# Kernel optimization log

Measured on AMD Instinct MI355X. Metric: run time of the kernel, lower is better.

The kernel has to match this reference:

```python
import jax, jax.numpy as jnp
import numpy as np

N_QUBITS = 10
DEPTH = 2
CNOT_PATTERN = [(i, i + 1) for i in range(N_QUBITS - 1)] + [(N_QUBITS - 1, 0)]

def _signs(n):
    # Pauli-Z eigenvalue (+1/-1) of each basis state for each wire; wire 0 = MSB
    idx = np.arange(2 ** n)
    bits = (idx[:, None] >> np.arange(n - 1, -1, -1)[None, :]) & 1
    return jnp.asarray(1.0 - 2.0 * bits, jnp.float32)  # [2^n, n]

SIGNS = _signs(N_QUBITS)

def _apply_rx(s, theta, wire):
    # s: [B, 2,2,...,2] complex; RX(theta) = [[c, -i s],[-i s, c]], c=cos(theta/2)
    s0 = jnp.take(s, 0, axis=wire + 1)
    s1 = jnp.take(s, 1, axis=wire + 1)
    c = jnp.cos(theta * 0.5)
    sn = jnp.sin(theta * 0.5)
    if c.ndim:  # per-batch angle -> broadcast over remaining wire axes
        shp = (-1,) + (1,) * (s0.ndim - 1)
        c = c.reshape(shp)
        sn = sn.reshape(shp)
    return jnp.stack([c * s0 - 1j * sn * s1, -1j * sn * s0 + c * s1], axis=wire + 1)

def _apply_cnot(s, src, tgt):
    # flip target wire on the src=1 subspace (X gate == flip of the size-2 axis)
    s0 = jnp.take(s, 0, axis=src + 1)
    s1 = jnp.take(s, 1, axis=src + 1)
    t_ax = tgt + 1 - (1 if tgt > src else 0)  # target axis after removing src axis
    s1 = jnp.flip(s1, axis=t_ax)
    return jnp.stack([s0, s1], axis=src + 1)

def _qgate(x, rx_params):
    # x: [B, n_qubits] data angles -> PauliZ expectations [B, n_qubits]
    B = x.shape[0]
    n = N_QUBITS
    s = jnp.zeros((B, 2 ** n), jnp.complex64).at[:, 0].set(1.0)
    s = s.reshape((B,) + (2,) * n)
    for w in range(n):
        s = _apply_rx(s, x[:, w], w)
    for _ in range(DEPTH):
        for w in range(n):
            s = _apply_rx(s, rx_params[w], w)
        for src, tgt in CNOT_PATTERN:
            s = _apply_cnot(s, src, tgt)
    probs = jnp.abs(s.reshape(B, -1)) ** 2  # [B, 2^n]
    return probs @ SIGNS  # [B, n]


def setup_inputs():
    key = jax.random.key(0)
    ks = jax.random.split(key, 10)
    T, B, D, H = 256, 256, 128, N_QUBITS
    fan_in = D + H
    sc = 1.0 / np.sqrt(fan_in)
    def lin(k1, k2):
        W = jax.random.uniform(k1, (H, fan_in), jnp.float32, -sc, sc)
        b = jax.random.uniform(k2, (H,), jnp.float32, -sc, sc)
        return W, b
    inputs = jax.random.normal(ks[0], (T, B, D), jnp.float32)
    rx_params = jax.random.normal(ks[1], (H,), jnp.float32)
    Wf, bf = lin(ks[2], ks[3])
    Wi, bi = lin(ks[4], ks[5])
    Wg, bg = lin(ks[6], ks[7])
    Wo, bo = lin(ks[8], ks[9])
    return dict(inputs=inputs, rx_params=rx_params, Wf=Wf, bf=bf, Wi=Wi, bi=bi,
                Wg=Wg, bg=bg, Wo=Wo, bo=bo)


def reference(inputs, rx_params, Wf, bf, Wi, bi, Wg, bg, Wo, bo):
    T, B, _ = inputs.shape
    H = N_QUBITS
    def step(carry, x_t):
        hx, cx = carry
        comb = jnp.concatenate([x_t, hx], axis=1)  # [B, D+H]
        f = jax.nn.sigmoid(_qgate(comb @ Wf.T + bf, rx_params))
        i = jax.nn.sigmoid(_qgate(comb @ Wi.T + bi, rx_params))
        g = jnp.tanh(_qgate(comb @ Wg.T + bg, rx_params))
        o = jax.nn.sigmoid(_qgate(comb @ Wo.T + bo, rx_params))
        cx = f * cx + i * g
        hx = o * jnp.tanh(cx)
        return (hx, cx), hx
    h0 = jnp.zeros((B, H), inputs.dtype)
    c0 = jnp.zeros((B, H), inputs.dtype)
    (hT, cT), ys = jax.lax.scan(step, (h0, c0), inputs)
    return ys, hT, cT
```

## Files before the change

kernel.cpp:

```cpp
#include <hip/hip_runtime.h>
#include <math.h>

#define T_STEPS 256
#define BATCH   256
#define DDIM    128
#define NH      10

typedef float v2f __attribute__((ext_vector_type(2)));

__device__ __forceinline__ v2f sp(float x){ v2f r; r.x = x; r.y = x; return r; }
#define PKFMA(a,b,c) __builtin_elementwise_fma((a),(b),(c))

template<int CTRL, int RMASK, int BMASK>
__device__ __forceinline__ float dppz(float x){
  return __int_as_float(__builtin_amdgcn_update_dpp(
      0, __float_as_int(x), CTRL, RMASK, BMASK, true));
}
template<int CTRL>
__device__ __forceinline__ float qperm(float x){
  int xi = __float_as_int(x);
  return __int_as_float(__builtin_amdgcn_update_dpp(xi, xi, CTRL, 0xF, 0xF, false));
}
__device__ __forceinline__ float red63(float v){
  v += dppz<0x111, 0xF, 0xF>(v);
  v += dppz<0x112, 0xF, 0xF>(v);
  v += dppz<0x114, 0xF, 0xE>(v);
  v += dppz<0x118, 0xF, 0xC>(v);
  v += dppz<0x142, 0xA, 0xF>(v);
  v += dppz<0x143, 0xC, 0xF>(v);
  return v;
}
__device__ __forceinline__ float wave_sum_b(float v){
  return __int_as_float(__builtin_amdgcn_readlane(__float_as_int(red63(v)), 63));
}
__device__ __forceinline__ float qp2(float x){ return qperm<0x4E>(x); }
__device__ __forceinline__ float qp1(float x){ return qperm<0xB1>(x); }

template<int CTRL, int RMASK, int BMASK>
__device__ __forceinline__ float lad_add(float v){ return v + dppz<CTRL,RMASK,BMASK>(v); }
template<int CTRL, int RMASK, int BMASK>
__device__ __forceinline__ float lad_sub(float v){ return dppz<CTRL,RMASK,BMASK>(v) - v; }

#define LAD0_A(v) lad_add<0x111,0xF,0xF>(v)
#define LAD0_S(v) lad_sub<0x111,0xF,0xF>(v)
#define LAD1_A(v) lad_add<0x112,0xF,0xF>(v)
#define LAD1_S(v) lad_sub<0x112,0xF,0xF>(v)
#define LAD2_A(v) lad_add<0x114,0xF,0xE>(v)
#define LAD2_S(v) lad_sub<0x114,0xF,0xE>(v)
#define LAD3_A(v) lad_add<0x118,0xF,0xC>(v)
#define LAD3_S(v) lad_sub<0x118,0xF,0xC>(v)
#define LAD4_A(v) lad_add<0x142,0xA,0xF>(v)
#define LAD4_S(v) lad_sub<0x142,0xA,0xF>(v)
#define LAD5_A(v) lad_add<0x143,0xC,0xF>(v)
#define LAD5_S(v) lad_sub<0x143,0xC,0xF>(v)

__device__ __forceinline__ float dsx32(float x){ return __shfl_xor(x, 32, 64); }
__device__ __forceinline__ float dsx16(float x){
  return __int_as_float(__builtin_amdgcn_ds_swizzle(__float_as_int(x), 0x401F));
}
__device__ __forceinline__ float dsx8(float x){
  return __int_as_float(__builtin_amdgcn_ds_swizzle(__float_as_int(x), 0x201F));
}
__device__ __forceinline__ float dsx4(float x){
  return __int_as_float(__builtin_amdgcn_ds_swizzle(__float_as_int(x), 0x101F));
}

#define NK 4

#define RX_LANE_PK(FETCH, cv, sv)                                              \
  { const v2f cc_ = sp(cv), ss_ = sp(sv);                                      \
    _Pragma("unroll")                                                          \
    for (int k = 0; k < NK; ++k){                                              \
      v2f oa, ob;                                                              \
      oa.x = FETCH(RE[k].x); oa.y = FETCH(RE[k].y);                            \
      ob.x = FETCH(IM[k].x); ob.y = FETCH(IM[k].y);                            \
      RE[k] = PKFMA(cc_, RE[k], ss_ * ob);                                     \
      IM[k] = PKFMA(cc_, IM[k], -(ss_ * oa));                                  \
    } }

template<int XB>
__device__ __forceinline__ void rx_reg_pk(float c, float s, v2f* RE, v2f* IM){
  const v2f cc = sp(c), ss = sp(s);
  v2f oR[NK], oI[NK];
  #pragma unroll
  for (int k = 0; k < NK; ++k){ oR[k] = RE[k]; oI[k] = IM[k]; }
  #pragma unroll
  for (int k = 0; k < NK; ++k){
    RE[k] = PKFMA(cc, oR[k],  ss * oI[k ^ XB]);
    IM[k] = PKFMA(cc, oI[k], -(ss * oR[k ^ XB]));
  }
}
__device__ __forceinline__ void rx_reg9_pk(float c, float s, v2f* RE, v2f* IM){
  const v2f cc = sp(c), ss = sp(s);
  #pragma unroll
  for (int k = 0; k < NK; ++k){
    v2f oa = __builtin_shufflevector(RE[k], RE[k], 1, 0);
    v2f ob = __builtin_shufflevector(IM[k], IM[k], 1, 0);
    RE[k] = PKFMA(cc, RE[k],  ss * ob);
    IM[k] = PKFMA(cc, IM[k], -(ss * oa));
  }
}

__global__ void __launch_bounds__(512)
__attribute__((amdgpu_waves_per_eu(2)))
qlstm_kernel(const float* __restrict__ inp, const float* __restrict__ rxp,
             const float* __restrict__ Wf, const float* __restrict__ bf,
             const float* __restrict__ Wi, const float* __restrict__ bi,
             const float* __restrict__ Wg, const float* __restrict__ bg,
             const float* __restrict__ Wo, const float* __restrict__ bo,
             float* __restrict__ out)
{
  const int b    = blockIdx.x;
  const int tid  = threadIdx.x;
  const int wv   = tid >> 6;
  const int g    = wv >> 1;
  const int half = wv & 1;
  const int lane = tid & 63;

  __shared__ float4 Sx[4][2][4][64];
  __shared__ float4 partv[2][64];
  __shared__ float2 csn[4][2][5];
  ((float*)partv)[tid] = 0.f;

  const float* Wp = (g == 0) ? Wf : (g == 1) ? Wi : (g == 2) ? Wg : Wo;
  const float* bp = (g == 0) ? bf : (g == 1) ? bi : (g == 2) ? bg : bo;

  const float WSC = 0.07957747154594767f;
  v2f WA[5], WB[5], WC[5];
  float bT[NH];
  #pragma unroll
  for (int j = 0; j < 5; ++j){
    const int w0 = 2*j, w1 = 2*j + 1;
    WA[j].x = WSC * Wp[w0*138 + lane];        WA[j].y = WSC * Wp[w1*138 + lane];
    WB[j].x = WSC * Wp[w0*138 + 64 + lane];   WB[j].y = WSC * Wp[w1*138 + 64 + lane];
    WC[j].x = (lane < NH) ? WSC * Wp[w0*138 + 128 + lane] : 0.f;
    WC[j].y = (lane < NH) ? WSC * Wp[w1*138 + 128 + lane] : 0.f;
  }
  #pragma unroll
  for (int w = 0; w < NH; ++w) bT[w] = WSC * (bp[w] + rxp[w]);

  float pc[NH], ps[NH];
  #pragma unroll
  for (int w = 0; w < NH; ++w){
    float th = 0.5f * rxp[w];
    pc[w] = cosf(th);
    ps[w] = sinf(th);
  }

  const int l5 = (lane>>5)&1, l4 = (lane>>4)&1, l3 = (lane>>3)&1;
  const int l2 = (lane>>2)&1, l1 = (lane>>1)&1, l0 = lane&1;
  const int pb2 = l4^l3, pb3 = l3^l2, pb4 = l2^l1, pb5 = l1^l0;
  const int a0 = l5, a1 = l5^l4;
  const int a6w = l0 ^ half;
  const int n_base = pb2 + pb3 + pb4 + pb5 + a6w;

  v2f CRE[NK], CIM[NK];
  #pragma unroll
  for (int r = 0; r < 2*NK; ++r){
    const int R0 = r&1, R1 = (r>>1)&1, R2 = (r>>2)&1;
    int k = (n_base + (a0^R0) + (a1^R0) + (half^R2) + (R2^R1) + (R1^R0)) & 3;
    float cr = (k==0) ? 1.f : (k==2) ? -1.f : 0.f;
    float ci = (k==1) ? -1.f : (k==3) ? 1.f : 0.f;
    if (R0){ CRE[r>>1].y = cr; CIM[r>>1].y = ci; }
    else   { CRE[r>>1].x = cr; CIM[r>>1].x = ci; }
  }

  const float sig = (lane == 0 || lane >= 6) ? -1.f : 1.f;

  float h = 0.f, c = 0.f;

  const float* x0 = inp + (size_t)b * DDIM;
  float xa = x0[lane];
  float xb = x0[64 + lane];

  __syncthreads();

  #pragma unroll 1
  for (int t = 0; t < T_STEPS; ++t){
    float xaC = xa, xbC = xb;
    if (t + 1 < T_STEPS){
      const float* nx = inp + ((size_t)(t+1) * BATCH + b) * DDIM;
      xa = nx[lane];
      xb = nx[64 + lane];
    }

    float cs[NH], sn[NH];
    {
      const v2f xav = sp(xaC), xbv = sp(xbC), hv = sp(h);
      if (half == 0){
        v2f p0 = PKFMA(xav, WA[0], PKFMA(xbv, WB[0], hv * WC[0]));
        v2f p1 = PKFMA(xav, WA[1], PKFMA(xbv, WB[1], hv * WC[1]));
        v2f p2 = PKFMA(xav, WA[2], PKFMA(xbv, WB[2], hv * WC[2]));
        float t0 = bT[0] + wave_sum_b(p0.x);
        float t1 = bT[1] + wave_sum_b(p0.y);
        float t2 = bT[2] + wave_sum_b(p1.x);
        float t3 = bT[3] + wave_sum_b(p1.y);
        float t4 = bT[4] + wave_sum_b(p2.x);
        cs[0] = __builtin_amdgcn_cosf(t0); sn[0] = __builtin_amdgcn_sinf(t0);
        cs[1] = __builtin_amdgcn_cosf(t1); sn[1] = __builtin_amdgcn_sinf(t1);
        cs[2] = __builtin_amdgcn_cosf(t2); sn[2] = __builtin_amdgcn_sinf(t2);
        cs[3] = __builtin_amdgcn_cosf(t3); sn[3] = __builtin_amdgcn_sinf(t3);
        cs[4] = __builtin_amdgcn_cosf(t4); sn[4] = __builtin_amdgcn_sinf(t4);
        if (lane == 0){
          csn[g][0][0] = make_float2(cs[0], sn[0]);
          csn[g][0][1] = make_float2(cs[1], sn[1]);
          csn[g][0][2] = make_float2(cs[2], sn[2]);
          csn[g][0][3] = make_float2(cs[3], sn[3]);
          csn[g][0][4] = make_float2(cs[4], sn[4]);
        }
      } else {
        v2f p2 = PKFMA(xav, WA[2], PKFMA(xbv, WB[2], hv * WC[2]));
        v2f p3 = PKFMA(xav, WA[3], PKFMA(xbv, WB[3], hv * WC[3]));
        v2f p4 = PKFMA(xav, WA[4], PKFMA(xbv, WB[4], hv * WC[4]));
        float t5 = bT[5] + wave_sum_b(p2.y);
        float t6 = bT[6] + wave_sum_b(p3.x);
        float t7 = bT[7] + wave_sum_b(p3.y);
        float t8 = bT[8] + wave_sum_b(p4.x);
        float t9 = bT[9] + wave_sum_b(p4.y);
        cs[5] = __builtin_amdgcn_cosf(t5); sn[5] = __builtin_amdgcn_sinf(t5);
        cs[6] = __builtin_amdgcn_cosf(t6); sn[6] = __builtin_amdgcn_sinf(t6);
        cs[7] = __builtin_amdgcn_cosf(t7); sn[7] = __builtin_amdgcn_sinf(t7);
        cs[8] = __builtin_amdgcn_cosf(t8); sn[8] = __builtin_amdgcn_sinf(t8);
        cs[9] = __builtin_amdgcn_cosf(t9); sn[9] = __builtin_amdgcn_sinf(t9);
        if (lane == 0){
          csn[g][1][0] = make_float2(cs[5], sn[5]);
          csn[g][1][1] = make_float2(cs[6], sn[6]);
          csn[g][1][2] = make_float2(cs[7], sn[7]);
          csn[g][1][3] = make_float2(cs[8], sn[8]);
          csn[g][1][4] = make_float2(cs[9], sn[9]);
        }
      }
    }
    __syncthreads();
    if (half == 0){
      float2 o0 = csn[g][1][0]; cs[5] = o0.x; sn[5] = o0.y;
      float2 o1 = csn[g][1][1]; cs[6] = o1.x; sn[6] = o1.y;
      float2 o2 = csn[g][1][2]; cs[7] = o2.x; sn[7] = o2.y;
      float2 o3 = csn[g][1][3]; cs[8] = o3.x; sn[8] = o3.y;
      float2 o4 = csn[g][1][4]; cs[9] = o4.x; sn[9] = o4.y;
    } else {
      float2 o0 = csn[g][0][0]; cs[0] = o0.x; sn[0] = o0.y;
      float2 o1 = csn[g][0][1]; cs[1] = o1.x; sn[1] = o1.y;
      float2 o2 = csn[g][0][2]; cs[2] = o2.x; sn[2] = o2.y;
      float2 o3 = csn[g][0][3]; cs[3] = o3.x; sn[3] = o3.y;
      float2 o4 = csn[g][0][4]; cs[4] = o4.x; sn[4] = o4.y;
    }

    float f2 = pb2 ? sn[2] : cs[2];
    float f3 = pb3 ? sn[3] : cs[3];
    float f4 = pb4 ? sn[4] : cs[4];
    float f5 = pb5 ? sn[5] : cs[5];
    float m2345 = ((f2*f3)*(f4*f5)) * (a6w ? sn[6] : cs[6]);

    float q0 = (a0 ? sn[0] : cs[0]) * (a1 ? sn[1] : cs[1]);
    float q1 = (a0 ? cs[0] : sn[0]) * (a1 ? cs[1] : sn[1]);
    v2f ZZ; ZZ.x = m2345 * q0; ZZ.y = m2345 * q1;

    float u7  = half ? sn[7] : cs[7];
    float u7b = half ? cs[7] : sn[7];
    float t78[4];
    t78[0] = u7  * cs[8];
    t78[1] = u7  * sn[8];
    t78[2] = u7b * sn[8];
    t78[3] = u7b * cs[8];

    v2f s9a; s9a.x = cs[9]; s9a.y = sn[9];
    v2f s9b; s9b.x = sn[9]; s9b.y = cs[9];

    v2f RE[NK], IM[NK];
    #pragma unroll
    for (int k = 0; k < NK; ++k){
      v2f M = (sp(t78[k]) * ((k & 1) ? s9b : s9a)) * ZZ;
      RE[k] = M * CRE[k];
      IM[k] = M * CIM[k];
    }

    RX_LANE_PK(dsx32, pc[0], ps[0])
    RX_LANE_PK(dsx16, pc[1], ps[1])
    RX_LANE_PK(dsx8,  pc[2], ps[2])
    RX_LANE_PK(dsx4,  pc[3], ps[3])
    RX_LANE_PK(qp2,   pc[4], ps[4])
    RX_LANE_PK(qp1,   pc[5], ps[5])
    rx_reg_pk<2>(pc[7], ps[7], RE, IM);
    rx_reg_pk<1>(pc[8], ps[8], RE, IM);
    rx_reg9_pk  (pc[9], ps[9], RE, IM);

    Sx[g][half][0][lane] = make_float4(RE[0].x, RE[0].y, RE[1].x, RE[1].y);
    Sx[g][half][1][lane] = make_float4(RE[2].x, RE[2].y, RE[3].x, RE[3].y);
    Sx[g][half][2][lane] = make_float4(IM[0].x, IM[0].y, IM[1].x, IM[1].y);
    Sx[g][half][3][lane] = make_float4(IM[2].x, IM[2].y, IM[3].x, IM[3].y);
    __syncthreads();
    {
      float4 pr0 = Sx[g][half^1][0][lane];
      float4 pr1 = Sx[g][half^1][1][lane];
      float4 pi0 = Sx[g][half^1][2][lane];
      float4 pi1 = Sx[g][half^1][3][lane];
      v2f PR[NK], PI[NK];
      PR[0].x = pr0.x; PR[0].y = pr0.y; PR[1].x = pr0.z; PR[1].y = pr0.w;
      PR[2].x = pr1.x; PR[2].y = pr1.y; PR[3].x = pr1.z; PR[3].y = pr1.w;
      PI[0].x = pi0.x; PI[0].y = pi0.y; PI[1].x = pi0.z; PI[1].y = pi0.w;
      PI[2].x = pi1.x; PI[2].y = pi1.y; PI[3].x = pi1.z; PI[3].y = pi1.w;
      const v2f c6 = sp(pc[6]), s6 = sp(ps[6]);
      #pragma unroll
      for (int k = 0; k < NK; ++k){
        RE[k] = PKFMA(c6, RE[k],  s6 * PI[k]);
        IM[k] = PKFMA(c6, IM[k], -(s6 * PR[k]));
      }
    }

    v2f Pk[NK];
    #pragma unroll
    for (int k = 0; k < NK; ++k) Pk[k] = PKFMA(RE[k], RE[k], IM[k] * IM[k]);
    float A0 = Pk[0].x + Pk[0].y, A1 = Pk[1].x + Pk[1].y;
    float A2 = Pk[2].x + Pk[2].y, A3 = Pk[3].x + Pk[3].y;
    float B0 = Pk[0].x - Pk[0].y, B1 = Pk[1].x - Pk[1].y;
    float B2 = Pk[2].x - Pk[2].y, B3 = Pk[3].x - Pk[3].y;
    float su = A0 + A1, sv = A2 + A3;
    float tot = su + sv;
    float q4  = su - sv;
    float q6  = (A0 - A1) - (A2 - A3);
    float q7  = (B0 - B1) - (B2 - B3);

    float a0p = LAD0_A(tot);
    float a0m = LAD0_S(tot);
    float b1pp = LAD1_A(a0p);
    float b1pm = LAD1_S(a0p);
    float b1mm = LAD1_S(a0m);
    float c2ppp = LAD2_A(b1pp);
    float c2ppm = LAD2_S(b1pp);
    float c2pmm = LAD2_S(b1pm);
    float c2mmm = LAD2_S(b1mm);
    float d1 = LAD3_A(c2ppp);
    float d2 = LAD3_S(c2ppp);
    float d3 = LAD3_S(c2ppm);
    float d4 = LAD3_S(c2pmm);
    float d5 = LAD3_S(c2mmm);
    float P1 = LAD5_S(LAD4_S(d1));
    float P2 = LAD5_S(LAD4_S(d2));
    float P3 = LAD5_S(LAD4_S(d3));
    float P4 = LAD5_S(LAD4_S(d4));
    float P5 = LAD5_S(LAD4_S(d5));
    float e = LAD0_S(q7);
    e = LAD1_S(e); e = LAD2_S(e); e = LAD3_S(e); e = LAD4_S(e);
    float P9 = LAD5_S(e);
    float P0 = LAD5_A(e);
    float f_ = LAD0_S(q4);
    f_ = LAD1_S(f_); f_ = LAD2_S(f_); f_ = LAD3_S(f_); f_ = LAD4_S(f_);
    float P7 = LAD5_S(f_);
    float g_ = LAD0_S(q6);
    g_ = LAD1_S(g_); g_ = LAD2_S(g_); g_ = LAD3_S(g_); g_ = LAD4_S(g_);
    float P8 = LAD5_S(g_);

    if (lane == 63){
      float vals[10] = {P0,P1,P2,P3,P4,P5,P5,P7,P8,P9};
      #pragma unroll
      for (int j = 0; j < 10; ++j)
        ((float*)&partv[half][j])[g] = vals[j];
    }
    __syncthreads();

    float4 eL = partv[0][lane];
    float4 eH = partv[1][lane];
    float E0 = fmaf(sig, eH.x, eL.x);
    float E1 = fmaf(sig, eH.y, eL.y);
    float E2 = fmaf(sig, eH.z, eL.z);
    float E3 = fmaf(sig, eH.w, eL.w);
    float fv = 1.f / (1.f + __expf(-E0));
    float iv = 1.f / (1.f + __expf(-E1));
    float e2g = __expf(2.f * E2);
    float gv = (e2g - 1.f) / (e2g + 1.f);
    float ov = 1.f / (1.f + __expf(-E3));
    c = fmaf(fv, c, iv * gv);
    float e2c = __expf(2.f * c);
    h = ov * ((e2c - 1.f) / (e2c + 1.f));

    if (wv == 0 && lane < NH)
      out[((size_t)t * BATCH + b) * NH + lane] = h;
  }

  if (wv == 0 && lane < NH){
    const size_t ysN = (size_t)T_STEPS * BATCH * NH;
    out[ysN + (size_t)b * NH + lane]                      = h;
    out[ysN + (size_t)BATCH * NH + (size_t)b * NH + lane] = c;
  }
}

extern "C" void kernel_launch(void* const* d_in, const int* in_sizes, int n_in,
                              void* d_out, int out_size, void* d_ws, size_t ws_size,
                              hipStream_t stream)
{
  qlstm_kernel<<<BATCH, 512, 0, stream>>>(
      (const float*)d_in[0], (const float*)d_in[1],
      (const float*)d_in[2], (const float*)d_in[3],
      (const float*)d_in[4], (const float*)d_in[5],
      (const float*)d_in[6], (const float*)d_in[7],
      (const float*)d_in[8], (const float*)d_in[9],
      (float*)d_out);
}
```

Baseline: 916.8 us.

## Split each gate's statevector across four waves with 1024-thread blocks

Each gate's 1024-amplitude state is now spread over four waves instead of two, so each lane keeps 8 amplitudes instead of 16. Qubits 6 and 7 become cross-wave and are applied together through one LDS exchange with the three partner waves. The per-wave angle projections use a shared shuffle-and-select reduction tree over 2–3 outputs instead of separate full wave sums. This halves per-wave register and ALU work and adds parallelism, at the cost of more LDS traffic and more threads per block in a serial recurrence.

```diff
diff --git a/kernel.cpp b/kernel.cpp
--- a/kernel.cpp
+++ b/kernel.cpp
@@ -7,7 +7,6 @@
 #define NH      10
 
 typedef float v2f __attribute__((ext_vector_type(2)));
-
 __device__ __forceinline__ v2f sp(float x){ v2f r; r.x = x; r.y = x; return r; }
 #define PKFMA(a,b,c) __builtin_elementwise_fma((a),(b),(c))
 
@@ -21,26 +20,17 @@
   int xi = __float_as_int(x);
   return __int_as_float(__builtin_amdgcn_update_dpp(xi, xi, CTRL, 0xF, 0xF, false));
 }
-__device__ __forceinline__ float red63(float v){
-  v += dppz<0x111, 0xF, 0xF>(v);
-  v += dppz<0x112, 0xF, 0xF>(v);
-  v += dppz<0x114, 0xF, 0xE>(v);
-  v += dppz<0x118, 0xF, 0xC>(v);
-  v += dppz<0x142, 0xA, 0xF>(v);
-  v += dppz<0x143, 0xC, 0xF>(v);
-  return v;
-}
-__device__ __forceinline__ float wave_sum_b(float v){
-  return __int_as_float(__builtin_amdgcn_readlane(__float_as_int(red63(v)), 63));
-}
 __device__ __forceinline__ float qp2(float x){ return qperm<0x4E>(x); }
 __device__ __forceinline__ float qp1(float x){ return qperm<0xB1>(x); }
 
-template<int CTRL, int RMASK, int BMASK>
+__device__ __forceinline__ float rdlane(float v, int l){
+  return __int_as_float(__builtin_amdgcn_readlane(__float_as_int(v), l));
+}
+
+template<int CTRL,int RMASK,int BMASK>
 __device__ __forceinline__ float lad_add(float v){ return v + dppz<CTRL,RMASK,BMASK>(v); }
-template<int CTRL, int RMASK, int BMASK>
+template<int CTRL,int RMASK,int BMASK>
 __device__ __forceinline__ float lad_sub(float v){ return dppz<CTRL,RMASK,BMASK>(v) - v; }
-
 #define LAD0_A(v) lad_add<0x111,0xF,0xF>(v)
 #define LAD0_S(v) lad_sub<0x111,0xF,0xF>(v)
 #define LAD1_A(v) lad_add<0x112,0xF,0xF>(v)
@@ -65,7 +55,39 @@
   return __int_as_float(__builtin_amdgcn_ds_swizzle(__float_as_int(x), 0x101F));
 }
 
-#define NK 4
+__device__ __forceinline__ void tree3(float v0, float v1, float v2,
+                                      int l5, int l4,
+                                      float& t0, float& t1, float& t2){
+  float a = v0 + dsx32(v0);
+  float b = v1 + dsx32(v1);
+  float c = v2 + dsx32(v2);
+  float m = l5 ? b : a;
+  m += dsx16(m);
+  c += dsx16(c);
+  float m2 = l4 ? c : m;
+  m2 += dsx8(m2);
+  m2 += dsx4(m2);
+  m2 += qp2(m2);
+  m2 += qp1(m2);
+  t0 = rdlane(m2, 0);
+  t1 = rdlane(m2, 32);
+  t2 = rdlane(m2, 16);
+}
+__device__ __forceinline__ void tree2(float v0, float v1, int l5,
+                                      float& t0, float& t1){
+  float a = v0 + dsx32(v0);
+  float b = v1 + dsx32(v1);
+  float m = l5 ? b : a;
+  m += dsx16(m);
+  m += dsx8(m);
+  m += dsx4(m);
+  m += qp2(m);
+  m += qp1(m);
+  t0 = rdlane(m, 0);
+  t1 = rdlane(m, 32);
+}
+
+#define NK 2
 
 #define RX_LANE_PK(FETCH, cv, sv)                                              \
   { const v2f cc_ = sp(cv), ss_ = sp(sv);                                      \
@@ -78,17 +100,13 @@
       IM[k] = PKFMA(cc_, IM[k], -(ss_ * oa));                                  \
     } }
 
-template<int XB>
-__device__ __forceinline__ void rx_reg_pk(float c, float s, v2f* RE, v2f* IM){
+__device__ __forceinline__ void rx_reg8_pk(float c, float s, v2f* RE, v2f* IM){
   const v2f cc = sp(c), ss = sp(s);
-  v2f oR[NK], oI[NK];
-  #pragma unroll
-  for (int k = 0; k < NK; ++k){ oR[k] = RE[k]; oI[k] = IM[k]; }
-  #pragma unroll
-  for (int k = 0; k < NK; ++k){
-    RE[k] = PKFMA(cc, oR[k],  ss * oI[k ^ XB]);
-    IM[k] = PKFMA(cc, oI[k], -(ss * oR[k ^ XB]));
-  }
+  v2f oR0 = RE[0], oI0 = IM[0], oR1 = RE[1], oI1 = IM[1];
+  RE[0] = PKFMA(cc, oR0,  ss * oI1);
+  IM[0] = PKFMA(cc, oI0, -(ss * oR1));
+  RE[1] = PKFMA(cc, oR1,  ss * oI0);
+  IM[1] = PKFMA(cc, oI1, -(ss * oR0));
 }
 __device__ __forceinline__ void rx_reg9_pk(float c, float s, v2f* RE, v2f* IM){
   const v2f cc = sp(c), ss = sp(s);
@@ -101,8 +119,8 @@
   }
 }
 
-__global__ void __launch_bounds__(512)
-__attribute__((amdgpu_waves_per_eu(2)))
+__global__ void __launch_bounds__(1024)
+__attribute__((amdgpu_waves_per_eu(4)))
 qlstm_kernel(const float* __restrict__ inp, const float* __restrict__ rxp,
              const float* __restrict__ Wf, const float* __restrict__ bf,
              const float* __restrict__ Wi, const float* __restrict__ bi,
@@ -113,31 +131,35 @@
   const int b    = blockIdx.x;
   const int tid  = threadIdx.x;
   const int wv   = tid >> 6;
-  const int g    = wv >> 1;
-  const int half = wv & 1;
+  const int g    = wv >> 2;
+  const int q    = wv & 3;
+  const int W1   = (q >> 1) & 1;
+  const int W0   = q & 1;
   const int lane = tid & 63;
 
-  __shared__ float4 Sx[4][2][4][64];
-  __shared__ float4 partv[2][64];
-  __shared__ float2 csn[4][2][5];
+  __shared__ float4 Sx[4][4][2][64];
+  __shared__ float4 partv[4][64];
+  __shared__ float4 csn4[4][5];
   ((float*)partv)[tid] = 0.f;
 
   const float* Wp = (g == 0) ? Wf : (g == 1) ? Wi : (g == 2) ? Wg : Wo;
   const float* bp = (g == 0) ? bf : (g == 1) ? bi : (g == 2) ? bg : bo;
 
+  const int cnt   = (q < 2) ? 3 : 2;
+  const int wbase = (q < 2) ? 3*q : 6 + 2*(q - 2);
+
   const float WSC = 0.07957747154594767f;
-  v2f WA[5], WB[5], WC[5];
-  float bT[NH];
+  float wa[3], wb[3], wc[3], bq[3];
   #pragma unroll
-  for (int j = 0; j < 5; ++j){
-    const int w0 = 2*j, w1 = 2*j + 1;
-    WA[j].x = WSC * Wp[w0*138 + lane];        WA[j].y = WSC * Wp[w1*138 + lane];
-    WB[j].x = WSC * Wp[w0*138 + 64 + lane];   WB[j].y = WSC * Wp[w1*138 + 64 + lane];
-    WC[j].x = (lane < NH) ? WSC * Wp[w0*138 + 128 + lane] : 0.f;
-    WC[j].y = (lane < NH) ? WSC * Wp[w1*138 + 128 + lane] : 0.f;
-  }
-  #pragma unroll
-  for (int w = 0; w < NH; ++w) bT[w] = WSC * (bp[w] + rxp[w]);
+  for (int j = 0; j < 3; ++j){
+    if (j < cnt){
+      const int w = wbase + j;
+      wa[j] = WSC * Wp[w*138 + lane];
+      wb[j] = WSC * Wp[w*138 + 64 + lane];
+      wc[j] = (lane < NH) ? WSC * Wp[w*138 + 128 + lane] : 0.f;
+      bq[j] = WSC * (bp[w] + rxp[w]);
+    } else { wa[j] = wb[j] = wc[j] = bq[j] = 0.f; }
+  }
 
   float pc[NH], ps[NH];
   #pragma unroll
@@ -146,26 +168,31 @@
     pc[w] = cosf(th);
     ps[w] = sinf(th);
   }
+  const float cc67 = pc[6]*pc[7], cs67 = pc[6]*ps[7];
+  const float sc67 = ps[6]*pc[7], ss67 = ps[6]*ps[7];
 
   const int l5 = (lane>>5)&1, l4 = (lane>>4)&1, l3 = (lane>>3)&1;
   const int l2 = (lane>>2)&1, l1 = (lane>>1)&1, l0 = lane&1;
   const int pb2 = l4^l3, pb3 = l3^l2, pb4 = l2^l1, pb5 = l1^l0;
   const int a0 = l5, a1 = l5^l4;
-  const int a6w = l0 ^ half;
+  const int a6w = l0 ^ W1;
+  const int w17 = W1 ^ W0;
   const int n_base = pb2 + pb3 + pb4 + pb5 + a6w;
 
   v2f CRE[NK], CIM[NK];
   #pragma unroll
   for (int r = 0; r < 2*NK; ++r){
-    const int R0 = r&1, R1 = (r>>1)&1, R2 = (r>>2)&1;
-    int k = (n_base + (a0^R0) + (a1^R0) + (half^R2) + (R2^R1) + (R1^R0)) & 3;
+    const int R0 = r&1, R1 = (r>>1)&1;
+    int k = (n_base + (a0^R0) + (a1^R0) + w17 + (W0^R1) + (R1^R0)) & 3;
     float cr = (k==0) ? 1.f : (k==2) ? -1.f : 0.f;
     float ci = (k==1) ? -1.f : (k==3) ? 1.f : 0.f;
     if (R0){ CRE[r>>1].y = cr; CIM[r>>1].y = ci; }
     else   { CRE[r>>1].x = cr; CIM[r>>1].x = ci; }
   }
 
-  const float sig = (lane == 0 || lane >= 6) ? -1.f : 1.f;
+  const float sg1 = (lane == 0 || lane >= 7) ? -1.f : 1.f;
+  const float sg2 = (lane == 0 || lane >= 6) ? -1.f : 1.f;
+  const float sg3 = (lane == 6) ? -1.f : 1.f;
 
   float h = 0.f, c = 0.f;
 
@@ -184,66 +211,34 @@
       xb = nx[64 + lane];
     }
 
+    {
+      float v0 = fmaf(xaC, wa[0], fmaf(xbC, wb[0], h * wc[0]));
+      float v1 = fmaf(xaC, wa[1], fmaf(xbC, wb[1], h * wc[1]));
+      float t0, t1, t2 = 0.f;
+      if (cnt == 3){
+        float v2 = fmaf(xaC, wa[2], fmaf(xbC, wb[2], h * wc[2]));
+        tree3(v0, v1, v2, l5, l4, t0, t1, t2);
+      } else {
+        tree2(v0, v1, l5, t0, t1);
+      }
+      t0 += bq[0]; t1 += bq[1]; t2 += bq[2];
+      float c0 = __builtin_amdgcn_cosf(t0), s0 = __builtin_amdgcn_sinf(t0);
+      float c1 = __builtin_amdgcn_cosf(t1), s1 = __builtin_amdgcn_sinf(t1);
+      float c2 = __builtin_amdgcn_cosf(t2), s2 = __builtin_amdgcn_sinf(t2);
+      if (lane == 0){
+        float2* c2p = (float2*)&csn4[g][0];
+        c2p[wbase]     = make_float2(c0, s0);
+        c2p[wbase + 1] = make_float2(c1, s1);
+        if (cnt == 3) c2p[wbase + 2] = make_float2(c2, s2);
+      }
+    }
+    __syncthreads();
     float cs[NH], sn[NH];
-    {
-      const v2f xav = sp(xaC), xbv = sp(xbC), hv = sp(h);
-      if (half == 0){
-        v2f p0 = PKFMA(xav, WA[0], PKFMA(xbv, WB[0], hv * WC[0]));
-        v2f p1 = PKFMA(xav, WA[1], PKFMA(xbv, WB[1], hv * WC[1]));
-        v2f p2 = PKFMA(xav, WA[2], PKFMA(xbv, WB[2], hv * WC[2]));
-        float t0 = bT[0] + wave_sum_b(p0.x);
-        float t1 = bT[1] + wave_sum_b(p0.y);
-        float t2 = bT[2] + wave_sum_b(p1.x);
-        float t3 = bT[3] + wave_sum_b(p1.y);
-        float t4 = bT[4] + wave_sum_b(p2.x);
-        cs[0] = __builtin_amdgcn_cosf(t0); sn[0] = __builtin_amdgcn_sinf(t0);
-        cs[1] = __builtin_amdgcn_cosf(t1); sn[1] = __builtin_amdgcn_sinf(t1);
-        cs[2] = __builtin_amdgcn_cosf(t2); sn[2] = __builtin_amdgcn_sinf(t2);
-        cs[3] = __builtin_amdgcn_cosf(t3); sn[3] = __builtin_amdgcn_sinf(t3);
-        cs[4] = __builtin_amdgcn_cosf(t4); sn[4] = __builtin_amdgcn_sinf(t4);
-        if (lane == 0){
-          csn[g][0][0] = make_float2(cs[0], sn[0]);
-          csn[g][0][1] = make_float2(cs[1], sn[1]);
-          csn[g][0][2] = make_float2(cs[2], sn[2]);
-          csn[g][0][3] = make_float2(cs[3], sn[3]);
-          csn[g][0][4] = make_float2(cs[4], sn[4]);
-        }
-      } else {
-        v2f p2 = PKFMA(xav, WA[2], PKFMA(xbv, WB[2], hv * WC[2]));
-        v2f p3 = PKFMA(xav, WA[3], PKFMA(xbv, WB[3], hv * WC[3]));
-        v2f p4 = PKFMA(xav, WA[4], PKFMA(xbv, WB[4], hv * WC[4]));
-        float t5 = bT[5] + wave_sum_b(p2.y);
-        float t6 = bT[6] + wave_sum_b(p3.x);
-        float t7 = bT[7] + wave_sum_b(p3.y);
-        float t8 = bT[8] + wave_sum_b(p4.x);
-        float t9 = bT[9] + wave_sum_b(p4.y);
-        cs[5] = __builtin_amdgcn_cosf(t5); sn[5] = __builtin_amdgcn_sinf(t5);
-        cs[6] = __builtin_amdgcn_cosf(t6); sn[6] = __builtin_amdgcn_sinf(t6);
-        cs[7] = __builtin_amdgcn_cosf(t7); sn[7] = __builtin_amdgcn_sinf(t7);
-        cs[8] = __builtin_amdgcn_cosf(t8); sn[8] = __builtin_amdgcn_sinf(t8);
-        cs[9] = __builtin_amdgcn_cosf(t9); sn[9] = __builtin_amdgcn_sinf(t9);
-        if (lane == 0){
-          csn[g][1][0] = make_float2(cs[5], sn[5]);
-          csn[g][1][1] = make_float2(cs[6], sn[6]);
-          csn[g][1][2] = make_float2(cs[7], sn[7]);
-          csn[g][1][3] = make_float2(cs[8], sn[8]);
-          csn[g][1][4] = make_float2(cs[9], sn[9]);
-        }
-      }
-    }
-    __syncthreads();
-    if (half == 0){
-      float2 o0 = csn[g][1][0]; cs[5] = o0.x; sn[5] = o0.y;
-      float2 o1 = csn[g][1][1]; cs[6] = o1.x; sn[6] = o1.y;
-      float2 o2 = csn[g][1][2]; cs[7] = o2.x; sn[7] = o2.y;
-      float2 o3 = csn[g][1][3]; cs[8] = o3.x; sn[8] = o3.y;
-      float2 o4 = csn[g][1][4]; cs[9] = o4.x; sn[9] = o4.y;
-    } else {
-      float2 o0 = csn[g][0][0]; cs[0] = o0.x; sn[0] = o0.y;
-      float2 o1 = csn[g][0][1]; cs[1] = o1.x; sn[1] = o1.y;
-      float2 o2 = csn[g][0][2]; cs[2] = o2.x; sn[2] = o2.y;
-      float2 o3 = csn[g][0][3]; cs[3] = o3.x; sn[3] = o3.y;
-      float2 o4 = csn[g][0][4]; cs[4] = o4.x; sn[4] = o4.y;
+    #pragma unroll
+    for (int j = 0; j < 5; ++j){
+      float4 cw = csn4[g][j];
+      cs[2*j]   = cw.x; sn[2*j]   = cw.y;
+      cs[2*j+1] = cw.z; sn[2*j+1] = cw.w;
     }
 
     float f2 = pb2 ? sn[2] : cs[2];
@@ -256,23 +251,18 @@
     float q1 = (a0 ? cs[0] : sn[0]) * (a1 ? cs[1] : sn[1]);
     v2f ZZ; ZZ.x = m2345 * q0; ZZ.y = m2345 * q1;
 
-    float u7  = half ? sn[7] : cs[7];
-    float u7b = half ? cs[7] : sn[7];
-    float t78[4];
-    t78[0] = u7  * cs[8];
-    t78[1] = u7  * sn[8];
-    t78[2] = u7b * sn[8];
-    t78[3] = u7b * cs[8];
-
+    float f7  = w17 ? sn[7] : cs[7];
+    float t8a = f7 * (W0 ? sn[8] : cs[8]);
+    float t8b = f7 * (W0 ? cs[8] : sn[8]);
     v2f s9a; s9a.x = cs[9]; s9a.y = sn[9];
     v2f s9b; s9b.x = sn[9]; s9b.y = cs[9];
 
     v2f RE[NK], IM[NK];
-    #pragma unroll
-    for (int k = 0; k < NK; ++k){
-      v2f M = (sp(t78[k]) * ((k & 1) ? s9b : s9a)) * ZZ;
-      RE[k] = M * CRE[k];
-      IM[k] = M * CIM[k];
+    {
+      v2f M0 = (sp(t8a) * s9a) * ZZ;
+      v2f M1 = (sp(t8b) * s9b) * ZZ;
+      RE[0] = M0 * CRE[0]; IM[0] = M0 * CIM[0];
+      RE[1] = M1 * CRE[1]; IM[1] = M1 * CIM[1];
     }
 
     RX_LANE_PK(dsx32, pc[0], ps[0])
@@ -281,45 +271,43 @@
     RX_LANE_PK(dsx4,  pc[3], ps[3])
     RX_LANE_PK(qp2,   pc[4], ps[4])
     RX_LANE_PK(qp1,   pc[5], ps[5])
-    rx_reg_pk<2>(pc[7], ps[7], RE, IM);
-    rx_reg_pk<1>(pc[8], ps[8], RE, IM);
-    rx_reg9_pk  (pc[9], ps[9], RE, IM);
-
-    Sx[g][half][0][lane] = make_float4(RE[0].x, RE[0].y, RE[1].x, RE[1].y);
-    Sx[g][half][1][lane] = make_float4(RE[2].x, RE[2].y, RE[3].x, RE[3].y);
-    Sx[g][half][2][lane] = make_float4(IM[0].x, IM[0].y, IM[1].x, IM[1].y);
-    Sx[g][half][3][lane] = make_float4(IM[2].x, IM[2].y, IM[3].x, IM[3].y);
+    rx_reg8_pk(pc[8], ps[8], RE, IM);
+    rx_reg9_pk(pc[9], ps[9], RE, IM);
+
+    Sx[g][q][0][lane] = make_float4(RE[0].x, RE[0].y, RE[1].x, RE[1].y);
+    Sx[g][q][1][lane] = make_float4(IM[0].x, IM[0].y, IM[1].x, IM[1].y);
     __syncthreads();
     {
-      float4 pr0 = Sx[g][half^1][0][lane];
-      float4 pr1 = Sx[g][half^1][1][lane];
-      float4 pi0 = Sx[g][half^1][2][lane];
-      float4 pi1 = Sx[g][half^1][3][lane];
-      v2f PR[NK], PI[NK];
-      PR[0].x = pr0.x; PR[0].y = pr0.y; PR[1].x = pr0.z; PR[1].y = pr0.w;
-      PR[2].x = pr1.x; PR[2].y = pr1.y; PR[3].x = pr1.z; PR[3].y = pr1.w;
-      PI[0].x = pi0.x; PI[0].y = pi0.y; PI[1].x = pi0.z; PI[1].y = pi0.w;
-      PI[2].x = pi1.x; PI[2].y = pi1.y; PI[3].x = pi1.z; PI[3].y = pi1.w;
-      const v2f c6 = sp(pc[6]), s6 = sp(ps[6]);
+      float4 r1 = Sx[g][q^1][0][lane], i1 = Sx[g][q^1][1][lane];
+      float4 r2 = Sx[g][q^2][0][lane], i2 = Sx[g][q^2][1][lane];
+      float4 r3 = Sx[g][q^3][0][lane], i3 = Sx[g][q^3][1][lane];
+      v2f R1v[2], I1v[2], R2v[2], I2v[2], R3v[2], I3v[2];
+      R1v[0].x = r1.x; R1v[0].y = r1.y; R1v[1].x = r1.z; R1v[1].y = r1.w;
+      I1v[0].x = i1.x; I1v[0].y = i1.y; I1v[1].x = i1.z; I1v[1].y = i1.w;
+      R2v[0].x = r2.x; R2v[0].y = r2.y; R2v[1].x = r2.z; R2v[1].y = r2.w;
+      I2v[0].x = i2.x; I2v[0].y = i2.y; I2v[1].x = i2.z; I2v[1].y = i2.w;
+      R3v[0].x = r3.x; R3v[0].y = r3.y; R3v[1].x = r3.z; R3v[1].y = r3.w;
+      I3v[0].x = i3.x; I3v[0].y = i3.y; I3v[1].x = i3.z; I3v[1].y = i3.w;
+      const v2f vcc = sp(cc67), vcs = sp(cs67), vsc = sp(sc67), vss = sp(ss67);
       #pragma unroll
       for (int k = 0; k < NK; ++k){
-        RE[k] = PKFMA(c6, RE[k],  s6 * PI[k]);
-        IM[k] = PKFMA(c6, IM[k], -(s6 * PR[k]));
+        v2f nre = PKFMA(vcc, RE[k],
+                  PKFMA(vcs, I1v[k],
+                  PKFMA(vsc, I2v[k], -(vss * R3v[k]))));
+        v2f nim = PKFMA(vcc, IM[k],
+                  -(PKFMA(vcs, R1v[k],
+                    PKFMA(vsc, R2v[k], vss * I3v[k]))));
+        RE[k] = nre; IM[k] = nim;
       }
     }
 
-    v2f Pk[NK];
-    #pragma unroll
-    for (int k = 0; k < NK; ++k) Pk[k] = PKFMA(RE[k], RE[k], IM[k] * IM[k]);
-    float A0 = Pk[0].x + Pk[0].y, A1 = Pk[1].x + Pk[1].y;
-    float A2 = Pk[2].x + Pk[2].y, A3 = Pk[3].x + Pk[3].y;
-    float B0 = Pk[0].x - Pk[0].y, B1 = Pk[1].x - Pk[1].y;
-    float B2 = Pk[2].x - Pk[2].y, B3 = Pk[3].x - Pk[3].y;
-    float su = A0 + A1, sv = A2 + A3;
-    float tot = su + sv;
-    float q4  = su - sv;
-    float q6  = (A0 - A1) - (A2 - A3);
-    float q7  = (B0 - B1) - (B2 - B3);
+    v2f Pk0 = PKFMA(RE[0], RE[0], IM[0]*IM[0]);
+    v2f Pk1 = PKFMA(RE[1], RE[1], IM[1]*IM[1]);
+    float A0 = Pk0.x + Pk0.y, A1 = Pk1.x + Pk1.y;
+    float B0 = Pk0.x - Pk0.y, B1 = Pk1.x - Pk1.y;
+    float tot = A0 + A1;
+    float qA  = A0 - A1;
+    float qB  = B0 - B1;
 
     float a0p = LAD0_A(tot);
     float a0m = LAD0_S(tot);
@@ -340,31 +328,30 @@
     float P3 = LAD5_S(LAD4_S(d3));
     float P4 = LAD5_S(LAD4_S(d4));
     float P5 = LAD5_S(LAD4_S(d5));
-    float e = LAD0_S(q7);
+    float e = LAD0_S(qB);
     e = LAD1_S(e); e = LAD2_S(e); e = LAD3_S(e); e = LAD4_S(e);
     float P9 = LAD5_S(e);
     float P0 = LAD5_A(e);
-    float f_ = LAD0_S(q4);
+    float f_ = LAD0_S(qA);
     f_ = LAD1_S(f_); f_ = LAD2_S(f_); f_ = LAD3_S(f_); f_ = LAD4_S(f_);
-    float P7 = LAD5_S(f_);
-    float g_ = LAD0_S(q6);
-    g_ = LAD1_S(g_); g_ = LAD2_S(g_); g_ = LAD3_S(g_); g_ = LAD4_S(g_);
-    float P8 = LAD5_S(g_);
+    float P8 = LAD5_S(f_);
 
     if (lane == 63){
-      float vals[10] = {P0,P1,P2,P3,P4,P5,P5,P7,P8,P9};
+      float vals[10] = {P0, P1, P2, P3, P4, P5, P5, P5, P8, P9};
       #pragma unroll
       for (int j = 0; j < 10; ++j)
-        ((float*)&partv[half][j])[g] = vals[j];
+        ((float*)&partv[q][j])[g] = vals[j];
     }
     __syncthreads();
 
-    float4 eL = partv[0][lane];
-    float4 eH = partv[1][lane];
-    float E0 = fmaf(sig, eH.x, eL.x);
-    float E1 = fmaf(sig, eH.y, eL.y);
-    float E2 = fmaf(sig, eH.z, eL.z);
-    float E3 = fmaf(sig, eH.w, eL.w);
+    float4 e0 = partv[0][lane];
+    float4 e1 = partv[1][lane];
+    float4 e2 = partv[2][lane];
+    float4 e3 = partv[3][lane];
+    float E0 = fmaf(sg3, e3.x, fmaf(sg2, e2.x, fmaf(sg1, e1.x, e0.x)));
+    float E1 = fmaf(sg3, e3.y, fmaf(sg2, e2.y, fmaf(sg1, e1.y, e0.y)));
+    float E2 = fmaf(sg3, e3.z, fmaf(sg2, e2.z, fmaf(sg1, e1.z, e0.z)));
+    float E3 = fmaf(sg3, e3.w, fmaf(sg2, e2.w, fmaf(sg1, e1.w, e0.w)));
     float fv = 1.f / (1.f + __expf(-E0));
     float iv = 1.f / (1.f + __expf(-E1));
     float e2g = __expf(2.f * E2);
@@ -389,7 +376,7 @@
                               void* d_out, int out_size, void* d_ws, size_t ws_size,
                               hipStream_t stream)
 {
-  qlstm_kernel<<<BATCH, 512, 0, stream>>>(
+  qlstm_kernel<<<BATCH, 1024, 0, stream>>>(
       (const float*)d_in[0], (const float*)d_in[1],
       (const float*)d_in[2], (const float*)d_in[3],
       (const float*)d_in[4], (const float*)d_in[5],
```

New measurement: 1.050 ms. +14.5%, slower.

## Precompute next-step input projections early and drop one barrier per step

Applied to the files above, without the earlier changes.

The input-dependent part of the gate pre-activations for step t+1 is now computed during step t, while the state vector is being exchanged. Each half-wave computes and publishes its 5 input dot products through shared memory at the existing barrier. The small h-dependent part (10 terms) is computed per lane with readlane broadcasts, and cos/sin are evaluated once per lane and then broadcast, which removes the csn shared exchange and one __syncthreads per step. The cost is extra readlanes per step and a reordering of the recurrence that shortens the serial critical path.

```diff
diff --git a/kernel.cpp b/kernel.cpp
--- a/kernel.cpp
+++ b/kernel.cpp
@@ -7,7 +7,6 @@
 #define NH      10
 
 typedef float v2f __attribute__((ext_vector_type(2)));
-
 __device__ __forceinline__ v2f sp(float x){ v2f r; r.x = x; r.y = x; return r; }
 #define PKFMA(a,b,c) __builtin_elementwise_fma((a),(b),(c))
 
@@ -30,17 +29,16 @@
   v += dppz<0x143, 0xC, 0xF>(v);
   return v;
 }
-__device__ __forceinline__ float wave_sum_b(float v){
-  return __int_as_float(__builtin_amdgcn_readlane(__float_as_int(red63(v)), 63));
+__device__ __forceinline__ float rdlane(float v, int l){
+  return __int_as_float(__builtin_amdgcn_readlane(__float_as_int(v), l));
 }
 __device__ __forceinline__ float qp2(float x){ return qperm<0x4E>(x); }
 __device__ __forceinline__ float qp1(float x){ return qperm<0xB1>(x); }
 
-template<int CTRL, int RMASK, int BMASK>
+template<int CTRL,int RMASK,int BMASK>
 __device__ __forceinline__ float lad_add(float v){ return v + dppz<CTRL,RMASK,BMASK>(v); }
-template<int CTRL, int RMASK, int BMASK>
+template<int CTRL,int RMASK,int BMASK>
 __device__ __forceinline__ float lad_sub(float v){ return dppz<CTRL,RMASK,BMASK>(v) - v; }
-
 #define LAD0_A(v) lad_add<0x111,0xF,0xF>(v)
 #define LAD0_S(v) lad_sub<0x111,0xF,0xF>(v)
 #define LAD1_A(v) lad_add<0x112,0xF,0xF>(v)
@@ -99,6 +97,17 @@
     RE[k] = PKFMA(cc, RE[k],  ss * ob);
     IM[k] = PKFMA(cc, IM[k], -(ss * oa));
   }
+}
+
+__device__ __forceinline__ void xdots(float xa, float xb,
+                                      const v2f* WA, const v2f* WB, float* s){
+  v2f xav = sp(xa), xbv = sp(xb);
+  v2f p0 = PKFMA(xav, WA[0], xbv * WB[0]);
+  v2f p1 = PKFMA(xav, WA[1], xbv * WB[1]);
+  v2f p2 = PKFMA(xav, WA[2], xbv * WB[2]);
+  s[0] = red63(p0.x); s[1] = red63(p0.y);
+  s[2] = red63(p1.x); s[3] = red63(p1.y);
+  s[4] = red63(p2.x);
 }
 
 __global__ void __launch_bounds__(512)
@@ -119,25 +128,38 @@
 
   __shared__ float4 Sx[4][2][4][64];
   __shared__ float4 partv[2][64];
-  __shared__ float2 csn[4][2][5];
+  __shared__ float xpub_s[4][16];
   ((float*)partv)[tid] = 0.f;
 
   const float* Wp = (g == 0) ? Wf : (g == 1) ? Wi : (g == 2) ? Wg : Wo;
   const float* bp = (g == 0) ? bf : (g == 1) ? bi : (g == 2) ? bg : bo;
 
   const float WSC = 0.07957747154594767f;
-  v2f WA[5], WB[5], WC[5];
-  float bT[NH];
-  #pragma unroll
-  for (int j = 0; j < 5; ++j){
-    const int w0 = 2*j, w1 = 2*j + 1;
-    WA[j].x = WSC * Wp[w0*138 + lane];        WA[j].y = WSC * Wp[w1*138 + lane];
-    WB[j].x = WSC * Wp[w0*138 + 64 + lane];   WB[j].y = WSC * Wp[w1*138 + 64 + lane];
-    WC[j].x = (lane < NH) ? WSC * Wp[w0*138 + 128 + lane] : 0.f;
-    WC[j].y = (lane < NH) ? WSC * Wp[w1*138 + 128 + lane] : 0.f;
-  }
-  #pragma unroll
-  for (int w = 0; w < NH; ++w) bT[w] = WSC * (bp[w] + rxp[w]);
+
+  const int wbase = half * 5;
+  v2f WA[3], WB[3];
+  float bq[5];
+  #pragma unroll
+  for (int k = 0; k < 5; ++k) bq[k] = WSC * (bp[wbase + k] + rxp[wbase + k]);
+  #pragma unroll
+  for (int j = 0; j < 3; ++j){
+    const int w0 = wbase + 2*j, w1 = wbase + 2*j + 1;
+    WA[j].x = WSC * Wp[w0*138 + lane];
+    WB[j].x = WSC * Wp[w0*138 + 64 + lane];
+    if (2*j + 1 < 5){
+      WA[j].y = WSC * Wp[w1*138 + lane];
+      WB[j].y = WSC * Wp[w1*138 + 64 + lane];
+    } else { WA[j].y = 0.f; WB[j].y = 0.f; }
+  }
+  float wCT[NH];
+  {
+    const int row = (lane < NH) ? lane : 0;
+    #pragma unroll
+    for (int j = 0; j < NH; ++j){
+      float v = WSC * Wp[row*138 + 128 + j];
+      wCT[j] = (lane < NH) ? v : 0.f;
+    }
+  }
 
   float pc[NH], ps[NH];
   #pragma unroll
@@ -173,11 +195,18 @@
   float xa = x0[lane];
   float xb = x0[64 + lane];
 
+  {
+    float sx[5];
+    xdots(xa, xb, WA, WB, sx);
+    if (lane == 63){
+      #pragma unroll
+      for (int k = 0; k < 5; ++k) xpub_s[g][wbase + k] = sx[k] + bq[k];
+    }
+  }
   __syncthreads();
 
   #pragma unroll 1
   for (int t = 0; t < T_STEPS; ++t){
-    float xaC = xa, xbC = xb;
     if (t + 1 < T_STEPS){
       const float* nx = inp + ((size_t)(t+1) * BATCH + b) * DDIM;
       xa = nx[lane];
@@ -186,64 +215,25 @@
 
     float cs[NH], sn[NH];
     {
-      const v2f xav = sp(xaC), xbv = sp(xbC), hv = sp(h);
-      if (half == 0){
-        v2f p0 = PKFMA(xav, WA[0], PKFMA(xbv, WB[0], hv * WC[0]));
-        v2f p1 = PKFMA(xav, WA[1], PKFMA(xbv, WB[1], hv * WC[1]));
-        v2f p2 = PKFMA(xav, WA[2], PKFMA(xbv, WB[2], hv * WC[2]));
-        float t0 = bT[0] + wave_sum_b(p0.x);
-        float t1 = bT[1] + wave_sum_b(p0.y);
-        float t2 = bT[2] + wave_sum_b(p1.x);
-        float t3 = bT[3] + wave_sum_b(p1.y);
-        float t4 = bT[4] + wave_sum_b(p2.x);
-        cs[0] = __builtin_amdgcn_cosf(t0); sn[0] = __builtin_amdgcn_sinf(t0);
-        cs[1] = __builtin_amdgcn_cosf(t1); sn[1] = __builtin_amdgcn_sinf(t1);
-        cs[2] = __builtin_amdgcn_cosf(t2); sn[2] = __builtin_amdgcn_sinf(t2);
-        cs[3] = __builtin_amdgcn_cosf(t3); sn[3] = __builtin_amdgcn_sinf(t3);
-        cs[4] = __builtin_amdgcn_cosf(t4); sn[4] = __builtin_amdgcn_sinf(t4);
-        if (lane == 0){
-          csn[g][0][0] = make_float2(cs[0], sn[0]);
-          csn[g][0][1] = make_float2(cs[1], sn[1]);
-          csn[g][0][2] = make_float2(cs[2], sn[2]);
-          csn[g][0][3] = make_float2(cs[3], sn[3]);
-          csn[g][0][4] = make_float2(cs[4], sn[4]);
-        }
-      } else {
-        v2f p2 = PKFMA(xav, WA[2], PKFMA(xbv, WB[2], hv * WC[2]));
-        v2f p3 = PKFMA(xav, WA[3], PKFMA(xbv, WB[3], hv * WC[3]));
-        v2f p4 = PKFMA(xav, WA[4], PKFMA(xbv, WB[4], hv * WC[4]));
-        float t5 = bT[5] + wave_sum_b(p2.y);
-        float t6 = bT[6] + wave_sum_b(p3.x);
-        float t7 = bT[7] + wave_sum_b(p3.y);
-        float t8 = bT[8] + wave_sum_b(p4.x);
-        float t9 = bT[9] + wave_sum_b(p4.y);
-        cs[5] = __builtin_amdgcn_cosf(t5); sn[5] = __builtin_amdgcn_sinf(t5);
-        cs[6] = __builtin_amdgcn_cosf(t6); sn[6] = __builtin_amdgcn_sinf(t6);
-        cs[7] = __builtin_amdgcn_cosf(t7); sn[7] = __builtin_amdgcn_sinf(t7);
-        cs[8] = __builtin_amdgcn_cosf(t8); sn[8] = __builtin_amdgcn_sinf(t8);
-        cs[9] = __builtin_amdgcn_cosf(t9); sn[9] = __builtin_amdgcn_sinf(t9);
-        if (lane == 0){
-          csn[g][1][0] = make_float2(cs[5], sn[5]);
-          csn[g][1][1] = make_float2(cs[6], sn[6]);
-          csn[g][1][2] = make_float2(cs[7], sn[7]);
-          csn[g][1][3] = make_float2(cs[8], sn[8]);
-          csn[g][1][4] = make_float2(cs[9], sn[9]);
-        }
+      float xr = xpub_s[g][lane & 15];
+      float hdA = rdlane(h, 0) * wCT[0];
+      float hdB = rdlane(h, 1) * wCT[1];
+      hdA = fmaf(rdlane(h, 2), wCT[2], hdA);
+      hdB = fmaf(rdlane(h, 3), wCT[3], hdB);
+      hdA = fmaf(rdlane(h, 4), wCT[4], hdA);
+      hdB = fmaf(rdlane(h, 5), wCT[5], hdB);
+      hdA = fmaf(rdlane(h, 6), wCT[6], hdA);
+      hdB = fmaf(rdlane(h, 7), wCT[7], hdB);
+      hdA = fmaf(rdlane(h, 8), wCT[8], hdA);
+      hdB = fmaf(rdlane(h, 9), wCT[9], hdB);
+      float th = xr + (hdA + hdB);
+      float cA = __builtin_amdgcn_cosf(th);
+      float sA = __builtin_amdgcn_sinf(th);
+      #pragma unroll
+      for (int w = 0; w < NH; ++w){
+        cs[w] = rdlane(cA, w);
+        sn[w] = rdlane(sA, w);
       }
-    }
-    __syncthreads();
-    if (half == 0){
-      float2 o0 = csn[g][1][0]; cs[5] = o0.x; sn[5] = o0.y;
-      float2 o1 = csn[g][1][1]; cs[6] = o1.x; sn[6] = o1.y;
-      float2 o2 = csn[g][1][2]; cs[7] = o2.x; sn[7] = o2.y;
-      float2 o3 = csn[g][1][3]; cs[8] = o3.x; sn[8] = o3.y;
-      float2 o4 = csn[g][1][4]; cs[9] = o4.x; sn[9] = o4.y;
-    } else {
-      float2 o0 = csn[g][0][0]; cs[0] = o0.x; sn[0] = o0.y;
-      float2 o1 = csn[g][0][1]; cs[1] = o1.x; sn[1] = o1.y;
-      float2 o2 = csn[g][0][2]; cs[2] = o2.x; sn[2] = o2.y;
-      float2 o3 = csn[g][0][3]; cs[3] = o3.x; sn[3] = o3.y;
-      float2 o4 = csn[g][0][4]; cs[4] = o4.x; sn[4] = o4.y;
     }
 
     float f2 = pb2 ? sn[2] : cs[2];
@@ -289,6 +279,10 @@
     Sx[g][half][1][lane] = make_float4(RE[2].x, RE[2].y, RE[3].x, RE[3].y);
     Sx[g][half][2][lane] = make_float4(IM[0].x, IM[0].y, IM[1].x, IM[1].y);
     Sx[g][half][3][lane] = make_float4(IM[2].x, IM[2].y, IM[3].x, IM[3].y);
+
+    float sx[5];
+    xdots(xa, xb, WA, WB, sx);
+
     __syncthreads();
     {
       float4 pr0 = Sx[g][half^1][0][lane];
@@ -356,6 +350,9 @@
       #pragma unroll
       for (int j = 0; j < 10; ++j)
         ((float*)&partv[half][j])[g] = vals[j];
+      #pragma unroll
+      for (int k = 0; k < 5; ++k)
+        xpub_s[g][wbase + k] = sx[k] + bq[k];
     }
     __syncthreads();
 
```

After: 879.6 us. 4.1% less time.
